# Optimization experiments

Hardware: AMD Instinct MI355X
Metric: run time of the kernel (lower is better)

The kernel has to match this reference:

```python
import jax, jax.numpy as jnp
import numpy as np

N_USERS = 100000
N_MOVIES = 100000
N_EDGES = 1000000
HIDDEN = 128


def setup_inputs() -> dict:
    key = jax.random.key(0)
    k1, k2, k3, k4, k5, k6, k7 = jax.random.split(key, 7)
    user_features = jax.random.normal(k1, (N_USERS, HIDDEN), dtype=jnp.float32)
    movie_features = jax.random.normal(k2, (N_MOVIES, HIDDEN), dtype=jnp.float32)
    src = jax.random.randint(k3, (N_EDGES,), 0, N_USERS, dtype=jnp.int64 if jax.config.jax_enable_x64 else jnp.int32)
    dst = jax.random.randint(k4, (N_EDGES,), 0, N_MOVIES, dtype=jnp.int64 if jax.config.jax_enable_x64 else jnp.int32)
    edge_index = jnp.stack([src, dst], axis=0)
    # Linear(2*HIDDEN, HIDDEN) params, torch-style init (kaiming uniform ~ U(-1/sqrt(fan_in), 1/sqrt(fan_in)))
    b1_bound = 1.0 / np.sqrt(2 * HIDDEN)
    W1 = jax.random.uniform(k5, (2 * HIDDEN, HIDDEN), minval=-b1_bound, maxval=b1_bound, dtype=jnp.float32)
    b1 = jax.random.uniform(k6, (HIDDEN,), minval=-b1_bound, maxval=b1_bound, dtype=jnp.float32)
    b2_bound = 1.0 / np.sqrt(HIDDEN)
    k8, k9 = jax.random.split(k7)
    W2 = jax.random.uniform(k8, (HIDDEN, 1), minval=-b2_bound, maxval=b2_bound, dtype=jnp.float32)
    b2 = jax.random.uniform(k9, (1,), minval=-b2_bound, maxval=b2_bound, dtype=jnp.float32)
    return {"user_features": user_features, "movie_features": movie_features,
            "edge_index": edge_index, "W1": W1, "b1": b1, "W2": W2, "b2": b2}


def reference(user_features, movie_features, edge_index, W1, b1, W2, b2):
    # Gather endpoint features per edge: [E, H] each
    u = user_features[edge_index[0]]
    m = movie_features[edge_index[1]]
    edge_feats = jnp.concatenate([u, m], axis=1)  # [E, 2H]
    h = jax.nn.relu(edge_feats @ W1 + b1)         # [E, H]
    out = h @ W2 + b2                             # [E, 1]
    return out.reshape(-1)
```

## Files before the change

kernel.cpp:

```cpp
#include <hip/hip_runtime.h>
#include <hip/hip_bf16.h>

typedef short s8v __attribute__((ext_vector_type(8)));
typedef float f4v __attribute__((ext_vector_type(4)));

__device__ __forceinline__ unsigned int bfround(float f) {
    unsigned int x = __float_as_uint(f);
    return (x + 0x7fffu + ((x >> 16) & 1u)) >> 16;
}
__device__ __forceinline__ unsigned int pkbf(float x, float y) {
    __hip_bfloat162 h = __float22bfloat162_rn(make_float2(x, y));
    return *(unsigned int*)&h;
}
__device__ __forceinline__ float i8f(unsigned int w, int k) {
    return (float)((int)(signed char)(w >> (8 * k)));
}

__global__ __launch_bounds__(256) void pack_w(const float* __restrict__ W1,
                                              uint4* __restrict__ WF)
{
    const int half = blockIdx.x;
    #pragma unroll
    for (int iter = 0; iter < 8; ++iter) {
        int idx  = iter * 256 + threadIdx.x;
        int lane = idx & 63;
        int t    = (idx >> 6) & 7;
        int c    = idx >> 9;
        int q = lane >> 4, m = lane & 15;
        unsigned int w[4];
        #pragma unroll
        for (int jj = 0; jj < 4; ++jj) {
            float lo = W1[(size_t)(half * 128 + c * 32 + q * 8 + 2 * jj    ) * 128 + t * 16 + m];
            float hi = W1[(size_t)(half * 128 + c * 32 + q * 8 + 2 * jj + 1) * 128 + t * 16 + m];
            w[jj] = bfround(lo) | (bfround(hi) << 16);
        }
        WF[(size_t)half * 2048 + idx] = make_uint4(w[0], w[1], w[2], w[3]);
    }
}

__global__ __launch_bounds__(384, 3) void proj_kernel(
    const float* __restrict__ userf, const float* __restrict__ movief,
    const uint4* __restrict__ WF, const float* __restrict__ b1,
    uint2* __restrict__ Pu, uint2* __restrict__ Pm,
    float* __restrict__ SU, float* __restrict__ SM,
    int ntiles, int bph)
{
    __shared__ uint4 wlds[2048];
    __shared__ uint4 alds[6][8][64];

    const int half = blockIdx.x >= bph;
    const int bid  = half ? blockIdx.x - bph : blockIdx.x;
    const float* __restrict__ feat = half ? movief : userf;
    uint2* __restrict__ P = half ? Pm : Pu;
    float* __restrict__ S = half ? SM : SU;
    const uint4* __restrict__ wfh = WF + (size_t)half * 2048;

    #pragma unroll
    for (int i = 0; i < 6; ++i) {
        int idx = i * 384 + threadIdx.x;
        if (idx < 2048) wlds[idx] = wfh[idx];
    }

    const int lane = threadIdx.x & 63;
    const int wv   = threadIdx.x >> 6;
    const int m    = lane & 15;
    const int q    = lane >> 4;

    const int wid = bid * 6 + wv;
    const int nw  = bph * 6;

    float bias_v[8];
    #pragma unroll
    for (int t = 0; t < 8; ++t)
        bias_v[t] = half ? b1[t * 16 + m] : 0.0f;

    const char* gfeat = (const char*)feat;
    const size_t lanebyte = ((size_t)m * 512 + (size_t)q * 32);

#define ISSUE_ALL(t_) do {                                                     \
        const char* gb_ = gfeat + (size_t)(t_) * 8192 + lanebyte;              \
        _Pragma("unroll")                                                      \
        for (int c_ = 0; c_ < 4; ++c_) {                                       \
            _Pragma("unroll")                                                  \
            for (int h_ = 0; h_ < 2; ++h_) {                                   \
                __builtin_amdgcn_global_load_lds(                              \
                    (const __attribute__((address_space(1))) void*)            \
                        (gb_ + c_ * 128 + h_ * 16),                            \
                    (__attribute__((address_space(3))) void*)&alds[wv][c_ * 2 + h_][0], \
                    16, 0, 0);                                                 \
            }                                                                  \
        }                                                                      \
    } while (0)

#define CVT2(p0, p1, dst) do {                                                 \
        uint4 aw_;                                                             \
        const float4 f0_ = *(const float4*)&(p0);                              \
        const float4 f1_ = *(const float4*)&(p1);                              \
        aw_.x = pkbf(f0_.x, f0_.y); aw_.y = pkbf(f0_.z, f0_.w);                \
        aw_.z = pkbf(f1_.x, f1_.y); aw_.w = pkbf(f1_.z, f1_.w);                \
        dst = *(const s8v*)&aw_;                                               \
    } while (0)

#define MFMA_C(c_, afv) do {                                                   \
        _Pragma("unroll")                                                      \
        for (int t_ = 0; t_ < 8; ++t_) {                                       \
            uint4 wf_ = wlds[((c_) * 8 + t_) * 64 + lane];                     \
            acc[t_] = __builtin_amdgcn_mfma_f32_16x16x32_bf16(                 \
                afv, *(const s8v*)&wf_, acc[t_], 0, 0, 0);                     \
        }                                                                      \
    } while (0)

#define WAIT_VM0()   do { asm volatile("s_waitcnt vmcnt(0)" ::: "memory");  \
                          __builtin_amdgcn_sched_barrier(0); } while (0)
#define WAIT_LGKM0() do { asm volatile("s_waitcnt lgkmcnt(0)" ::: "memory"); \
                          __builtin_amdgcn_sched_barrier(0); } while (0)

    int tile = wid;
    if (tile < ntiles) ISSUE_ALL(tile);

    __syncthreads();

    while (tile < ntiles) {
        const int nxt = tile + nw;

        f4v acc[8];
        #pragma unroll
        for (int t = 0; t < 8; ++t)
            acc[t] = (f4v){bias_v[t], bias_v[t], bias_v[t], bias_v[t]};

        WAIT_VM0();
        uint4 p0 = alds[wv][0][lane], p1 = alds[wv][1][lane];
        uint4 p2 = alds[wv][2][lane], p3 = alds[wv][3][lane];
        uint4 p4 = alds[wv][4][lane], p5 = alds[wv][5][lane];
        uint4 p6 = alds[wv][6][lane], p7 = alds[wv][7][lane];
        s8v af0, af1, af2, af3;
        CVT2(p0, p1, af0);
        CVT2(p2, p3, af1);
        CVT2(p4, p5, af2);
        CVT2(p6, p7, af3);
        WAIT_LGKM0();
        if (nxt < ntiles) ISSUE_ALL(nxt);

        MFMA_C(0, af0);
        MFMA_C(1, af1);
        MFMA_C(2, af2);
        MFMA_C(3, af3);

        #pragma unroll
        for (int r = 0; r < 4; ++r) {
            float mx = 0.0f;
            #pragma unroll
            for (int t = 0; t < 8; ++t) mx = fmaxf(mx, fabsf(acc[t][r]));
            #pragma unroll
            for (int off = 1; off < 16; off <<= 1)
                mx = fmaxf(mx, __shfl_xor(mx, off, 64));
            float inv = mx > 0.0f ? 127.0f / mx : 0.0f;

            unsigned int lo = 0, hi = 0;
            #pragma unroll
            for (int t = 0; t < 4; ++t) {
                lo |= ((unsigned int)(__float2int_rn(acc[t][r]     * inv) & 0xff)) << (8 * t);
                hi |= ((unsigned int)(__float2int_rn(acc[t + 4][r] * inv) & 0xff)) << (8 * t);
            }
            int row = tile * 16 + q * 4 + r;
            P[(size_t)row * 16 + m] = make_uint2(lo, hi);
            if (m == 0) S[row] = mx * (1.0f / 127.0f);
        }

        tile = nxt;
    }
#undef ISSUE_ALL
#undef CVT2
#undef MFMA_C
#undef WAIT_VM0
#undef WAIT_LGKM0
}

__global__ __launch_bounds__(256) void edge_kernel(
    const int* __restrict__ src, const int* __restrict__ dst,
    const uint2* __restrict__ Pu, const uint2* __restrict__ Pm,
    const float* __restrict__ SU, const float* __restrict__ SM,
    const float* __restrict__ W2, const float* __restrict__ b2,
    float* __restrict__ out)
{
    const int lane = threadIdx.x & 63;
    const int L    = lane & 15;
    const int g    = lane >> 4;
    const int eg   = (blockIdx.x * 4 + (threadIdx.x >> 6)) * 16 + g * 4;

    float w2v[8];
    #pragma unroll
    for (int j = 0; j < 8; ++j) w2v[j] = W2[j * 16 + L];

    int si[4], di[4];
    #pragma unroll
    for (int i = 0; i < 4; ++i) { si[i] = src[eg + i]; di[i] = dst[eg + i]; }

    uint2 pu[4], pm[4];
    float scu[4], scm[4];
    #pragma unroll
    for (int i = 0; i < 4; ++i) {
        pu[i] = Pu[(size_t)si[i] * 16 + L];
        pm[i] = Pm[(size_t)di[i] * 16 + L];
        scu[i] = SU[si[i]];
        scm[i] = SM[di[i]];
    }

    float res[4];
    #pragma unroll
    for (int i = 0; i < 4; ++i) {
        const unsigned int uw[2] = {pu[i].x, pu[i].y};
        const unsigned int mw[2] = {pm[i].x, pm[i].y};
        float acc = 0.0f;
        #pragma unroll
        for (int v = 0; v < 2; ++v) {
            #pragma unroll
            for (int k = 0; k < 4; ++k) {
                float h = fmaf(scu[i], i8f(uw[v], k), scm[i] * i8f(mw[v], k));
                acc = fmaf(fmaxf(h, 0.0f), w2v[v * 4 + k], acc);
            }
        }
        #pragma unroll
        for (int off = 1; off < 16; off <<= 1)
            acc += __shfl_xor(acc, off, 64);
        res[i] = acc;
    }

    if (L == 0) {
        float bb = b2[0];
        *(float4*)(out + eg) = make_float4(res[0] + bb, res[1] + bb, res[2] + bb, res[3] + bb);
    }
}

extern "C" void kernel_launch(void* const* d_in, const int* in_sizes, int n_in,
                              void* d_out, int out_size, void* d_ws, size_t ws_size,
                              hipStream_t stream) {
    const float* userf  = (const float*)d_in[0];
    const float* movief = (const float*)d_in[1];
    const int*   eidx   = (const int*)d_in[2];
    const float* W1     = (const float*)d_in[3];
    const float* b1     = (const float*)d_in[4];
    const float* W2     = (const float*)d_in[5];
    const float* b2     = (const float*)d_in[6];
    float* out = (float*)d_out;

    const int NU = in_sizes[0] / 128;
    const int NM = in_sizes[1] / 128;
    const int E  = in_sizes[2] / 2;

    uint2* Pu = (uint2*)d_ws;
    uint2* Pm = Pu + (size_t)NU * 16;
    float* SU = (float*)(Pm + (size_t)NM * 16);
    float* SM = SU + NU;
    uint4* WF = (uint4*)(SM + NM);

    const int ntiles = NU / 16;
    const int bph    = 256;

    pack_w<<<2, 256, 0, stream>>>(W1, WF);
    proj_kernel<<<2 * bph, 384, 0, stream>>>(userf, movief, WF, b1, Pu, Pm, SU, SM, ntiles, bph);
    edge_kernel<<<E / 64, 256, 0, stream>>>(eidx, eidx + E, Pu, Pm, SU, SM, W2, b2, out);
}
```

Baseline: 184.6 us.

## Coalesce feature-row loads into LDS with XOR swizzle and reshape proj launch

```diff
diff --git a/kernel.cpp b/kernel.cpp
--- a/kernel.cpp
+++ b/kernel.cpp
@@ -38,7 +38,7 @@
     }
 }
 
-__global__ __launch_bounds__(384, 3) void proj_kernel(
+__global__ __launch_bounds__(256, 2) void proj_kernel(
     const float* __restrict__ userf, const float* __restrict__ movief,
     const uint4* __restrict__ WF, const float* __restrict__ b1,
     uint2* __restrict__ Pu, uint2* __restrict__ Pm,
@@ -46,7 +46,7 @@
     int ntiles, int bph)
 {
     __shared__ uint4 wlds[2048];
-    __shared__ uint4 alds[6][8][64];
+    __shared__ uint4 alds[4][512];
 
     const int half = blockIdx.x >= bph;
     const int bid  = half ? blockIdx.x - bph : blockIdx.x;
@@ -56,41 +56,41 @@
     const uint4* __restrict__ wfh = WF + (size_t)half * 2048;
 
     #pragma unroll
-    for (int i = 0; i < 6; ++i) {
-        int idx = i * 384 + threadIdx.x;
-        if (idx < 2048) wlds[idx] = wfh[idx];
-    }
+    for (int i = 0; i < 8; ++i)
+        wlds[i * 256 + threadIdx.x] = wfh[i * 256 + threadIdx.x];
 
     const int lane = threadIdx.x & 63;
     const int wv   = threadIdx.x >> 6;
     const int m    = lane & 15;
     const int q    = lane >> 4;
 
-    const int wid = bid * 6 + wv;
-    const int nw  = bph * 6;
+    const int wid = bid * 4 + wv;
+    const int nw  = bph * 4;
 
     float bias_v[8];
     #pragma unroll
     for (int t = 0; t < 8; ++t)
         bias_v[t] = half ? b1[t * 16 + m] : 0.0f;
 
-    const char* gfeat = (const char*)feat;
-    const size_t lanebyte = ((size_t)m * 512 + (size_t)q * 32);
+    const char* gfeat  = (const char*)feat;
+    const int   rhalf  = lane >> 5;
+    const int   l31x16 = (lane & 31) * 16;
 
 #define ISSUE_ALL(t_) do {                                                     \
-        const char* gb_ = gfeat + (size_t)(t_) * 8192 + lanebyte;              \
+        const char* gb_ = gfeat + (size_t)(t_) * 8192;                         \
         _Pragma("unroll")                                                      \
-        for (int c_ = 0; c_ < 4; ++c_) {                                       \
-            _Pragma("unroll")                                                  \
-            for (int h_ = 0; h_ < 2; ++h_) {                                   \
-                __builtin_amdgcn_global_load_lds(                              \
-                    (const __attribute__((address_space(1))) void*)            \
-                        (gb_ + c_ * 128 + h_ * 16),                            \
-                    (__attribute__((address_space(3))) void*)&alds[wv][c_ * 2 + h_][0], \
-                    16, 0, 0);                                                 \
-            }                                                                  \
+        for (int j_ = 0; j_ < 8; ++j_) {                                       \
+            const int r_ = 2 * j_ + rhalf;                                     \
+            const size_t so_ = (size_t)r_ * 512 + (size_t)(l31x16 ^ ((r_ & 7) << 4)); \
+            __builtin_amdgcn_global_load_lds(                                  \
+                (const __attribute__((address_space(1))) void*)(gb_ + so_),    \
+                (__attribute__((address_space(3))) void*)&alds[wv][j_ * 64],   \
+                16, 0, 0);                                                     \
         }                                                                      \
     } while (0)
+
+    const int swz = m & 7;
+#define APULL(c_, h_) alds[wv][m * 32 + (((c_) * 8 + q * 2 + (h_)) ^ swz)]
 
 #define CVT2(p0, p1, dst) do {                                                 \
         uint4 aw_;                                                             \
@@ -129,10 +129,10 @@
             acc[t] = (f4v){bias_v[t], bias_v[t], bias_v[t], bias_v[t]};
 
         WAIT_VM0();
-        uint4 p0 = alds[wv][0][lane], p1 = alds[wv][1][lane];
-        uint4 p2 = alds[wv][2][lane], p3 = alds[wv][3][lane];
-        uint4 p4 = alds[wv][4][lane], p5 = alds[wv][5][lane];
-        uint4 p6 = alds[wv][6][lane], p7 = alds[wv][7][lane];
+        uint4 p0 = APULL(0, 0), p1 = APULL(0, 1);
+        uint4 p2 = APULL(1, 0), p3 = APULL(1, 1);
+        uint4 p4 = APULL(2, 0), p5 = APULL(2, 1);
+        uint4 p6 = APULL(3, 0), p7 = APULL(3, 1);
         s8v af0, af1, af2, af3;
         CVT2(p0, p1, af0);
         CVT2(p2, p3, af1);
@@ -170,6 +170,7 @@
         tile = nxt;
     }
 #undef ISSUE_ALL
+#undef APULL
 #undef CVT2
 #undef MFMA_C
 #undef WAIT_VM0
@@ -255,9 +256,9 @@
     uint4* WF = (uint4*)(SM + NM);
 
     const int ntiles = NU / 16;
-    const int bph    = 256;
+    const int bph    = 512;
 
     pack_w<<<2, 256, 0, stream>>>(W1, WF);
-    proj_kernel<<<2 * bph, 384, 0, stream>>>(userf, movief, WF, b1, Pu, Pm, SU, SM, ntiles, bph);
+    proj_kernel<<<2 * bph, 256, 0, stream>>>(userf, movief, WF, b1, Pu, Pm, SU, SM, ntiles, bph);
     edge_kernel<<<E / 64, 256, 0, stream>>>(eidx, eidx + E, Pu, Pm, SU, SM, W2, b2, out);
 }
```

New measurement: 181.5 us. About the same (-1.7%).
